# Optimization experiments

Measured on AMD Instinct MI355X. Metric: run time of the kernel, lower is better.

The kernel has to match this reference:

```python
import jax, jax.numpy as jnp
import numpy as np

EPS = 1e-12
LORA_RANK = 16

def setup_inputs() -> dict:
    key = jax.random.key(0)
    ks = jax.random.split(key, 7)
    bs, sq, din, dout = 8, 2048, 2048, 2048
    n_tasks, n_splits, n_skills, r = 32, 1, 8, LORA_RANK
    return {
        'x': jax.random.normal(ks[0], (bs, sq, din), dtype=jnp.float32),
        'W': jax.random.normal(ks[1], (dout, din), dtype=jnp.float32) * (1.0 / np.sqrt(din)),
        'b': jax.random.normal(ks[2], (dout,), dtype=jnp.float32) * 0.02,
        'module_logits': jax.random.normal(ks[3], (n_tasks, n_splits * n_skills), dtype=jnp.float32) * 0.001,
        'A': jax.random.normal(ks[4], (n_splits, n_skills, din // n_splits, r), dtype=jnp.float32) * 0.02,
        'B': jax.random.normal(ks[5], (n_splits, n_skills, r, dout // n_splits), dtype=jnp.float32) * 0.02,
        'tasks': jax.random.randint(ks[6], (bs,), 0, n_tasks),
    }

def reference(x, W, b, module_logits, A, B, tasks):
    bs, sq, din = x.shape
    n_splits, n_skills, _, r = A.shape
    dout = W.shape[0]
    # Polytropon selector (eval mode): sigmoid + normalize over skills
    probs = jax.nn.sigmoid(module_logits[tasks]).reshape(bs, n_splits, n_skills)
    probs = probs / (probs.sum(-1, keepdims=True) + EPS)  # [bs, p, t]
    # WeightedSum combinor: per-example skill mixture of LoRA params
    A_c = jnp.einsum('bpt,ptir->bpir', probs, A)  # [bs, p, din/p, r]
    B_c = jnp.einsum('bpt,ptro->bpro', probs, B)  # [bs, p, r, dout/p]
    # LoRA forward: reshape to per-example [din, r] and [r, dout]
    A_r = A_c.reshape(bs, din, r)
    B_r = jnp.transpose(B_c, (0, 2, 1, 3)).reshape(bs, r, dout)
    lora = jnp.einsum('bsr,bro->bso', jnp.einsum('bsi,bir->bsr', x, A_r), B_r)
    base = jnp.einsum('bsi,oi->bso', x, W) + b
    return base + lora * (1.0 / r)
```

## Files before the change

### kernel.cpp

```cpp
#include <hip/hip_runtime.h>

typedef __attribute__((ext_vector_type(4))) float f32x4;
typedef __attribute__((ext_vector_type(8))) short bf16x8;

__device__ __forceinline__ unsigned short f2b(float f) {
  unsigned u = __float_as_uint(f);
  u = (u + 0x7FFFu + ((u >> 16) & 1u)) >> 16;
  return (unsigned short)u;
}

#define BAR() asm volatile("s_barrier" ::: "memory")
#define VMCNT(N) asm volatile("s_waitcnt vmcnt(" #N ")" ::: "memory")

__global__ void combine_wconv_kernel(const float* __restrict__ logits,
                                     const int*   __restrict__ tasks,
                                     const float* __restrict__ A,
                                     const float* __restrict__ B,
                                     const float* __restrict__ W,
                                     unsigned short* __restrict__ Art,
                                     unsigned short* __restrict__ Brt,
                                     unsigned short* __restrict__ Wb)
{
  int blk = blockIdx.x;
  int tid = threadIdx.x;
  if (blk >= 64) {
    int idx0 = (blk - 64) * 256 + tid;
    #pragma unroll
    for (int c = 0; c < 32; ++c) {
      size_t i = ((size_t)idx0 + (size_t)c * 32768) * 4;
      f32x4 v = *(const f32x4*)(W + i);
      ushort4 o;
      o.x = f2b(v.x); o.y = f2b(v.y); o.z = f2b(v.z); o.w = f2b(v.w);
      *(ushort4*)(Wb + i) = o;
    }
    return;
  }
  int idx = blk * 256 + tid;
  int b = idx >> 11;
  int i = idx & 2047;
  int task = tasks[b];
  float p[8]; float s = 0.f;
  #pragma unroll
  for (int t = 0; t < 8; ++t) {
    float l = logits[task * 8 + t];
    float e = 1.f / (1.f + __expf(-l));
    p[t] = e; s += e;
  }
  float inv = 1.f / (s + 1e-12f);
  #pragma unroll
  for (int t = 0; t < 8; ++t) p[t] *= inv;

  float ar[16];
  #pragma unroll
  for (int r = 0; r < 16; ++r) ar[r] = 0.f;
  for (int t = 0; t < 8; ++t) {
    const float* ap = A + ((size_t)t * 2048 + i) * 16;
    float pt = p[t];
    #pragma unroll
    for (int r = 0; r < 16; ++r) ar[r] += pt * ap[r];
  }
  #pragma unroll
  for (int r = 0; r < 16; ++r)
    Art[((size_t)b * 16 + r) * 2048 + i] = f2b(ar[r]);

  float br[16];
  #pragma unroll
  for (int r = 0; r < 16; ++r) br[r] = 0.f;
  for (int t = 0; t < 8; ++t) {
    float pt = p[t];
    #pragma unroll
    for (int r = 0; r < 16; ++r) br[r] += pt * B[((size_t)t * 16 + r) * 2048 + i];
  }
  #pragma unroll
  for (int r = 0; r < 16; ++r)
    Brt[((size_t)b * 2048 + i) * 16 + r] = f2b(br[r] * 0.0625f);
}

__global__ void prep_kernel(const float* __restrict__ x,
                            const unsigned short* __restrict__ Art,
                            unsigned short* __restrict__ xb,
                            unsigned short* __restrict__ xa)
{
  __shared__ float red[4][16][16];
  int blk = blockIdx.x;
  int tid = threadIdx.x;
  int lane = tid & 63, wv = tid >> 6;
  int lr = lane & 15, hi = lane >> 4;
  int rowbase = blk * 16;
  int batch = rowbase >> 11;
  int row = rowbase + lr;
  f32x4 acc; acc.x = 0.f; acc.y = 0.f; acc.z = 0.f; acc.w = 0.f;
  const float* xrow = x + (size_t)row * 2048 + wv * 512 + hi * 8;
  unsigned short* xbrow = xb + (size_t)row * 2048 + wv * 512 + hi * 8;
  const unsigned short* artrow = Art + ((size_t)batch * 16 + lr) * 2048 + wv * 512 + hi * 8;
  #pragma unroll
  for (int ks = 0; ks < 16; ++ks) {
    f32x4 v0 = *(const f32x4*)(xrow + ks * 32);
    f32x4 v1 = *(const f32x4*)(xrow + ks * 32 + 4);
    bf16x8 av;
    av[0] = (short)f2b(v0.x); av[1] = (short)f2b(v0.y);
    av[2] = (short)f2b(v0.z); av[3] = (short)f2b(v0.w);
    av[4] = (short)f2b(v1.x); av[5] = (short)f2b(v1.y);
    av[6] = (short)f2b(v1.z); av[7] = (short)f2b(v1.w);
    *(bf16x8*)(xbrow + ks * 32) = av;
    bf16x8 bv = *(const bf16x8*)(artrow + ks * 32);
    acc = __builtin_amdgcn_mfma_f32_16x16x32_bf16(av, bv, acc, 0, 0, 0);
  }
  #pragma unroll
  for (int j = 0; j < 4; ++j) red[wv][hi * 4 + j][lr] = acc[j];
  __syncthreads();
  int rr = tid >> 4, cc = tid & 15;
  float s = red[0][rr][cc] + red[1][rr][cc] + red[2][rr][cc] + red[3][rr][cc];
  xa[(size_t)(rowbase + rr) * 16 + cc] = f2b(s);
}

__global__ __launch_bounds__(512, 4)
void gemm_kernel(const unsigned short* __restrict__ xb,
                 const unsigned short* __restrict__ Wb,
                 const float* __restrict__ bias,
                 const unsigned short* __restrict__ xa,
                 const unsigned short* __restrict__ Brt,
                 float* __restrict__ out)
{
  __shared__ __align__(16) char lds[49152];
  const int tid = threadIdx.x;
  const int lane = tid & 63;
  const int wv = tid >> 6;
  const int wr = wv >> 2, wc = wv & 3;
  const int lr = lane & 15, hi = lane >> 4;
  const int hi16 = hi * 16;

  const int bid = blockIdx.x;
  const int tn = bid & 7, tm = bid >> 3;
  const int rowbase = tm * 128, colbase = tn * 256;

  const int row0 = tid >> 3;
  const int scb_e = (((tid & 7) * 16) ^ ((row0 & 7) << 4)) >> 1;

#define GL16(LDSOFF, GPTR) \
  __builtin_amdgcn_global_load_lds((const __attribute__((address_space(1))) unsigned int*)(GPTR), \
      (__attribute__((address_space(3))) unsigned int*)(lds + (LDSOFF)), 16, 0, 0)

#define STAGE_ALL(KOFF) { \
  const unsigned short* ga_ = xb + (size_t)(rowbase + row0) * 2048 + (KOFF) + scb_e; \
  GL16(tid * 16, ga_); \
  GL16(8192 + tid * 16, ga_ + 64 * 2048); \
  const unsigned short* gb_ = Wb + (size_t)(colbase + row0) * 2048 + (KOFF) + scb_e; \
  GL16(16384 + tid * 16, gb_); \
  GL16(16384 + 8192 + tid * 16, gb_ + 64 * 2048); \
  GL16(16384 + 16384 + tid * 16, gb_ + 128 * 2048); \
  GL16(16384 + 24576 + tid * 16, gb_ + 192 * 2048); \
}

  f32x4 acc[4][4];
  #pragma unroll
  for (int i = 0; i < 4; ++i)
    #pragma unroll
    for (int n = 0; n < 4; ++n) { acc[i][n].x = 0.f; acc[i][n].y = 0.f; acc[i][n].z = 0.f; acc[i][n].w = 0.f; }

  bf16x8 a[4][2];

  for (int kt = 0; kt < 32; ++kt) {
    STAGE_ALL(kt * 64);
    VMCNT(0);
    BAR();

    #pragma unroll
    for (int mf = 0; mf < 4; ++mf) {
      int ar = wr * 64 + mf * 16 + lr;
      #pragma unroll
      for (int kk = 0; kk < 2; ++kk)
        a[mf][kk] = *(const bf16x8*)(lds + ar * 128 + ((kk * 64 + hi16) ^ ((ar & 7) << 4)));
    }
    #pragma unroll
    for (int nf = 0; nf < 4; ++nf) {
      int br = wc * 64 + nf * 16 + lr;
      bf16x8 b0 = *(const bf16x8*)(lds + 16384 + br * 128 + ((hi16) ^ ((br & 7) << 4)));
      bf16x8 b1 = *(const bf16x8*)(lds + 16384 + br * 128 + ((64 + hi16) ^ ((br & 7) << 4)));
      __builtin_amdgcn_s_setprio(1);
      #pragma unroll
      for (int mf = 0; mf < 4; ++mf) {
        acc[mf][nf] = __builtin_amdgcn_mfma_f32_16x16x32_bf16(a[mf][0], b0, acc[mf][nf], 0, 0, 0);
        acc[mf][nf] = __builtin_amdgcn_mfma_f32_16x16x32_bf16(a[mf][1], b1, acc[mf][nf], 0, 0, 0);
      }
      __builtin_amdgcn_s_setprio(0);
    }
    BAR();
  }

  const int batch = rowbase >> 11;
  bf16x8 zf = (bf16x8)(short)0;
  bf16x8 ea[4], eb[4];
  #pragma unroll
  for (int i = 0; i < 4; ++i) {
    if (hi < 2)
      ea[i] = *(const bf16x8*)(xa + (size_t)(rowbase + wr * 64 + i * 16 + lr) * 16 + hi * 8);
    else
      ea[i] = zf;
  }
  #pragma unroll
  for (int n = 0; n < 4; ++n) {
    if (hi < 2)
      eb[n] = *(const bf16x8*)(Brt + ((size_t)batch * 2048 + colbase + wc * 64 + n * 16 + lr) * 16 + hi * 8);
    else
      eb[n] = zf;
  }
  #pragma unroll
  for (int i = 0; i < 4; ++i)
    #pragma unroll
    for (int n = 0; n < 4; ++n)
      acc[i][n] = __builtin_amdgcn_mfma_f32_16x16x32_bf16(ea[i], eb[n], acc[i][n], 0, 0, 0);

  #pragma unroll
  for (int n = 0; n < 4; ++n) {
    int col = colbase + wc * 64 + n * 16 + lr;
    float bbv = bias[col];
    #pragma unroll
    for (int i = 0; i < 4; ++i) {
      int r0 = rowbase + wr * 64 + i * 16 + hi * 4;
      #pragma unroll
      for (int j = 0; j < 4; ++j)
        out[(size_t)(r0 + j) * 2048 + col] = acc[i][n][j] + bbv;
    }
  }
#undef GL16
#undef STAGE_ALL
}

extern "C" void kernel_launch(void* const* d_in, const int* in_sizes, int n_in,
                              void* d_out, int out_size, void* d_ws, size_t ws_size,
                              hipStream_t stream) {
  const float* x      = (const float*)d_in[0];
  const float* W      = (const float*)d_in[1];
  const float* bias   = (const float*)d_in[2];
  const float* logits = (const float*)d_in[3];
  const float* A      = (const float*)d_in[4];
  const float* B      = (const float*)d_in[5];
  const int*   tasks  = (const int*)d_in[6];
  float* out = (float*)d_out;

  char* ws = (char*)d_ws;
  unsigned short* xb  = (unsigned short*)(ws);
  unsigned short* Wb  = (unsigned short*)(ws + 67108864);
  unsigned short* xa  = (unsigned short*)(ws + 67108864 + 8388608);
  unsigned short* Art = (unsigned short*)(ws + 67108864 + 8388608 + 524288);
  unsigned short* Brt = (unsigned short*)(ws + 67108864 + 8388608 + 1048576);

  combine_wconv_kernel<<<192, 256, 0, stream>>>(logits, tasks, A, B, W, Art, Brt, Wb);
  prep_kernel<<<1024, 256, 0, stream>>>(x, Art, xb, xa);
  gemm_kernel<<<1024, 512, 0, stream>>>(xb, Wb, bias, xa, Brt, out);
}
```

Baseline: 200.7 us.

## Enlarge GEMM tile to 256x256 with double-buffered B and direct A loads

Result: slower. 229.2 us (+14.2%).

```diff
diff --git a/kernel.cpp b/kernel.cpp
--- a/kernel.cpp
+++ b/kernel.cpp
@@ -11,6 +11,7 @@
 
 #define BAR() asm volatile("s_barrier" ::: "memory")
 #define VMCNT(N) asm volatile("s_waitcnt vmcnt(" #N ")" ::: "memory")
+#define LGKM0() { asm volatile("s_waitcnt lgkmcnt(0)" ::: "memory"); __builtin_amdgcn_sched_barrier(0); }
 
 __global__ void combine_wconv_kernel(const float* __restrict__ logits,
                                      const int*   __restrict__ tasks,
@@ -114,7 +115,7 @@
   xa[(size_t)(rowbase + rr) * 16 + cc] = f2b(s);
 }
 
-__global__ __launch_bounds__(512, 4)
+__global__ __launch_bounds__(512, 2)
 void gemm_kernel(const unsigned short* __restrict__ xb,
                  const unsigned short* __restrict__ Wb,
                  const float* __restrict__ bias,
@@ -122,75 +123,96 @@
                  const unsigned short* __restrict__ Brt,
                  float* __restrict__ out)
 {
-  __shared__ __align__(16) char lds[49152];
+  __shared__ __align__(16) char lds[65536];
   const int tid = threadIdx.x;
   const int lane = tid & 63;
   const int wv = tid >> 6;
-  const int wr = wv >> 2, wc = wv & 3;
+  const int wr = wv >> 1, wc = wv & 1;
   const int lr = lane & 15, hi = lane >> 4;
   const int hi16 = hi * 16;
 
   const int bid = blockIdx.x;
   const int tn = bid & 7, tm = bid >> 3;
-  const int rowbase = tm * 128, colbase = tn * 256;
+  const int rowbase = tm * 256, colbase = tn * 256;
 
   const int row0 = tid >> 3;
   const int scb_e = (((tid & 7) * 16) ^ ((row0 & 7) << 4)) >> 1;
+
+  const unsigned short* agb = xb + (size_t)(rowbase + wr * 64 + lr) * 2048 + hi * 8;
 
 #define GL16(LDSOFF, GPTR) \
   __builtin_amdgcn_global_load_lds((const __attribute__((address_space(1))) unsigned int*)(GPTR), \
       (__attribute__((address_space(3))) unsigned int*)(lds + (LDSOFF)), 16, 0, 0)
 
-#define STAGE_ALL(KOFF) { \
-  const unsigned short* ga_ = xb + (size_t)(rowbase + row0) * 2048 + (KOFF) + scb_e; \
-  GL16(tid * 16, ga_); \
-  GL16(8192 + tid * 16, ga_ + 64 * 2048); \
-  const unsigned short* gb_ = Wb + (size_t)(colbase + row0) * 2048 + (KOFF) + scb_e; \
-  GL16(16384 + tid * 16, gb_); \
-  GL16(16384 + 8192 + tid * 16, gb_ + 64 * 2048); \
-  GL16(16384 + 16384 + tid * 16, gb_ + 128 * 2048); \
-  GL16(16384 + 24576 + tid * 16, gb_ + 192 * 2048); \
-}
-
-  f32x4 acc[4][4];
+#define STAGE_B(DBUF, KOFF) { \
+  const unsigned short* g_ = Wb + (size_t)(colbase + row0) * 2048 + (KOFF) + scb_e; \
+  GL16((DBUF)*32768 + tid*16, g_); \
+  GL16((DBUF)*32768 + 8192 + tid*16, g_ + 64*2048); \
+  GL16((DBUF)*32768 + 16384 + tid*16, g_ + 128*2048); \
+  GL16((DBUF)*32768 + 24576 + tid*16, g_ + 192*2048); \
+}
+
+#define RD_B16(BUF) \
+  _Pragma("unroll") \
+  for (int nf = 0; nf < 8; ++nf) { \
+    int br_ = wc*128 + nf*16 + lr; \
+    _Pragma("unroll") \
+    for (int kk = 0; kk < 2; ++kk) \
+      bb[nf][kk] = *(const bf16x8*)(lds + (BUF)*32768 + br_*128 + ((kk*64 + hi16) ^ ((br_&7)<<4))); \
+  }
+
+#define LOADA_MF(MF, KOFF) { \
+  a[MF][0] = *(const bf16x8*)(agb + (size_t)(MF)*16*2048 + (KOFF)); \
+  a[MF][1] = *(const bf16x8*)(agb + (size_t)(MF)*16*2048 + (KOFF) + 32); \
+}
+
+#define MM_MF(MF) \
+  __builtin_amdgcn_s_setprio(1); \
+  _Pragma("unroll") \
+  for (int nf = 0; nf < 8; ++nf) \
+    _Pragma("unroll") \
+    for (int kk = 0; kk < 2; ++kk) \
+      acc[MF][nf] = __builtin_amdgcn_mfma_f32_16x16x32_bf16( \
+          a[MF][kk], bb[nf][kk], acc[MF][nf], 0, 0, 0); \
+  __builtin_amdgcn_s_setprio(0);
+
+  f32x4 acc[4][8];
   #pragma unroll
   for (int i = 0; i < 4; ++i)
     #pragma unroll
-    for (int n = 0; n < 4; ++n) { acc[i][n].x = 0.f; acc[i][n].y = 0.f; acc[i][n].z = 0.f; acc[i][n].w = 0.f; }
-
-  bf16x8 a[4][2];
+    for (int n = 0; n < 8; ++n) { acc[i][n].x = 0.f; acc[i][n].y = 0.f; acc[i][n].z = 0.f; acc[i][n].w = 0.f; }
+
+  bf16x8 a[4][2], bb[8][2];
+
+  STAGE_B(0, 0);
+  LOADA_MF(0, 0); LOADA_MF(1, 0); LOADA_MF(2, 0); LOADA_MF(3, 0);
+  VMCNT(8);
+  BAR();
 
   for (int kt = 0; kt < 32; ++kt) {
-    STAGE_ALL(kt * 64);
-    VMCNT(0);
-    BAR();
-
-    #pragma unroll
-    for (int mf = 0; mf < 4; ++mf) {
-      int ar = wr * 64 + mf * 16 + lr;
-      #pragma unroll
-      for (int kk = 0; kk < 2; ++kk)
-        a[mf][kk] = *(const bf16x8*)(lds + ar * 128 + ((kk * 64 + hi16) ^ ((ar & 7) << 4)));
-    }
-    #pragma unroll
-    for (int nf = 0; nf < 4; ++nf) {
-      int br = wc * 64 + nf * 16 + lr;
-      bf16x8 b0 = *(const bf16x8*)(lds + 16384 + br * 128 + ((hi16) ^ ((br & 7) << 4)));
-      bf16x8 b1 = *(const bf16x8*)(lds + 16384 + br * 128 + ((64 + hi16) ^ ((br & 7) << 4)));
-      __builtin_amdgcn_s_setprio(1);
-      #pragma unroll
-      for (int mf = 0; mf < 4; ++mf) {
-        acc[mf][nf] = __builtin_amdgcn_mfma_f32_16x16x32_bf16(a[mf][0], b0, acc[mf][nf], 0, 0, 0);
-        acc[mf][nf] = __builtin_amdgcn_mfma_f32_16x16x32_bf16(a[mf][1], b1, acc[mf][nf], 0, 0, 0);
-      }
-      __builtin_amdgcn_s_setprio(0);
-    }
+    const int buf = kt & 1, nbuf = buf ^ 1;
+    const int k1 = (kt + 1) * 64;
+
+    RD_B16(buf);
+    if (kt < 31) STAGE_B(nbuf, k1);
+    LGKM0();
+
+    MM_MF(0);
+    if (kt < 31) LOADA_MF(0, k1);
+    MM_MF(1);
+    if (kt < 31) LOADA_MF(1, k1);
+    MM_MF(2);
+    if (kt < 31) LOADA_MF(2, k1);
+    MM_MF(3);
+    if (kt < 31) LOADA_MF(3, k1);
+
+    if (kt < 31) { VMCNT(8); }
     BAR();
   }
 
   const int batch = rowbase >> 11;
   bf16x8 zf = (bf16x8)(short)0;
-  bf16x8 ea[4], eb[4];
+  bf16x8 ea[4], eb[8];
   #pragma unroll
   for (int i = 0; i < 4; ++i) {
     if (hi < 2)
@@ -199,21 +221,21 @@
       ea[i] = zf;
   }
   #pragma unroll
-  for (int n = 0; n < 4; ++n) {
+  for (int n = 0; n < 8; ++n) {
     if (hi < 2)
-      eb[n] = *(const bf16x8*)(Brt + ((size_t)batch * 2048 + colbase + wc * 64 + n * 16 + lr) * 16 + hi * 8);
+      eb[n] = *(const bf16x8*)(Brt + ((size_t)batch * 2048 + colbase + wc * 128 + n * 16 + lr) * 16 + hi * 8);
     else
       eb[n] = zf;
   }
   #pragma unroll
   for (int i = 0; i < 4; ++i)
     #pragma unroll
-    for (int n = 0; n < 4; ++n)
+    for (int n = 0; n < 8; ++n)
       acc[i][n] = __builtin_amdgcn_mfma_f32_16x16x32_bf16(ea[i], eb[n], acc[i][n], 0, 0, 0);
 
   #pragma unroll
-  for (int n = 0; n < 4; ++n) {
-    int col = colbase + wc * 64 + n * 16 + lr;
+  for (int n = 0; n < 8; ++n) {
+    int col = colbase + wc * 128 + n * 16 + lr;
     float bbv = bias[col];
     #pragma unroll
     for (int i = 0; i < 4; ++i) {
@@ -224,7 +246,10 @@
     }
   }
 #undef GL16
-#undef STAGE_ALL
+#undef STAGE_B
+#undef RD_B16
+#undef LOADA_MF
+#undef MM_MF
 }
 
 extern "C" void kernel_launch(void* const* d_in, const int* in_sizes, int n_in,
@@ -248,5 +273,5 @@
 
   combine_wconv_kernel<<<192, 256, 0, stream>>>(logits, tasks, A, B, W, Art, Brt, Wb);
   prep_kernel<<<1024, 256, 0, stream>>>(x, Art, xb, xa);
-  gemm_kernel<<<1024, 512, 0, stream>>>(xb, Wb, bias, xa, Brt, out);
-}
+  gemm_kernel<<<512, 512, 0, stream>>>(xb, Wb, bias, xa, Brt, out);
+}
```
